# Kernel tuning notes

Hardware: AMD Instinct MI355X
Metric: run time of the kernel (lower is better)

## Reference

```python
import jax, jax.numpy as jnp
import numpy as np

H = 768; R = 16; L = 3; NS = 128; NQ = 128


def setup_inputs():
    key = jax.random.key(0)
    ks = iter(jax.random.split(key, 40))
    def w(shape, s=0.02):
        return (s * jax.random.normal(next(ks), shape)).astype(jnp.float32)
    return {
        "support_features": jax.random.normal(next(ks), (NS, H), jnp.float32),
        "support_labels": jax.random.randint(next(ks), (NS,), 0, 3),
        "query_features": jax.random.normal(next(ks), (NQ, H), jnp.float32),
        "sim_w1": w((H, 2 * H)), "sim_b1": jnp.zeros((H,), jnp.float32),
        "sim_w2": w((R, H)), "sim_b2": jnp.zeros((R,), jnp.float32),
        "div_w1": w((H, 2 * H)), "div_b1": jnp.zeros((H,), jnp.float32),
        "div_w2": w((R, H)), "div_b2": jnp.zeros((R,), jnp.float32),
        "rel_w": w((L, R, H, H)), "rel_b": jnp.zeros((L, R, H), jnp.float32),
        "agg_w1": w((L, H, 2 * H)), "agg_b1": jnp.zeros((L, H), jnp.float32),
        "agg_w2": w((L, H, H)), "agg_b2": jnp.zeros((L, H), jnp.float32),
        "ln_g": jnp.ones((L, H), jnp.float32), "ln_b": jnp.zeros((L, H), jnp.float32),
        "cls_w1": w((H // 2, H)), "cls_b1": jnp.zeros((H // 2,), jnp.float32),
        "cls_w2": w((3, H // 2)), "cls_b2": jnp.zeros((3,), jnp.float32),
    }


def _symmetrize(F):
    # torch loop fills [i,j] and [j,i] with value computed from pair (min(i,j), max(i,j)); diag stays 0
    N = F.shape[0]
    idx = jnp.arange(N)
    lower = (idx[:, None] > idx[None, :])
    Fs = jnp.where(lower[:, :, None], jnp.swapaxes(F, 0, 1), F)
    off = (idx[:, None] != idx[None, :]).astype(F.dtype)
    return Fs * off[:, :, None]


def _relations(x, w1, b1, w2, b2, diversity):
    h = x.shape[1]
    wa, wb = w1[:, :h], w1[:, h:]  # split concat([a,b]) @ w1^T into two matmuls
    pa = x @ wa.T                  # [N,H], contribution of first element (x_i)
    if diversity:
        d = jnp.abs(x[:, None, :] - x[None, :, :])   # [N,N,H]
        hid = jax.nn.relu(pa[:, None, :] + d @ wb.T + b1)
    else:
        pb = x @ wb.T
        hid = jax.nn.relu(pa[:, None, :] + pb[None, :, :] + b1)
    logits = hid @ w2.T + b2       # [N,N,R]
    return _symmetrize(jax.nn.softmax(logits, axis=-1))


def _layer_norm(y, g, b):
    mu = y.mean(-1, keepdims=True)
    var = ((y - mu) ** 2).mean(-1, keepdims=True)
    return (y - mu) / jnp.sqrt(var + 1e-5) * g + b


def _prop_layer(x, C, rw, rb, aw1, ab1, aw2, ab2, g, b):
    N = x.shape[0]
    T = jnp.einsum('jh,rkh->jrk', x, rw) + rb       # per-relation transform [N,R,H]
    msg = jnp.einsum('ijr,jrk->ik', C, T) / (N - 1)  # mean over N-1 neighbors (diag of C is 0)
    comb = jnp.concatenate([x, msg], axis=-1)
    agg = jax.nn.relu(comb @ aw1.T + ab1) @ aw2.T + ab2
    return _layer_norm(agg + x, g, b)


def reference(support_features, support_labels, query_features,
              sim_w1, sim_b1, sim_w2, sim_b2,
              div_w1, div_b1, div_w2, div_b2,
              rel_w, rel_b, agg_w1, agg_b1, agg_w2, agg_b2, ln_g, ln_b,
              cls_w1, cls_b1, cls_w2, cls_b2):
    all_x = jnp.concatenate([support_features, query_features], axis=0)
    sim = _relations(all_x, sim_w1, sim_b1, sim_w2, sim_b2, diversity=False)
    div = _relations(all_x, div_w1, div_b1, div_w2, div_b2, diversity=True)
    C = (sim + div) * 0.5
    x = all_x
    for l in range(L):
        x = _prop_layer(x, C, rel_w[l], rel_b[l], agg_w1[l], agg_b1[l],
                        agg_w2[l], agg_b2[l], ln_g[l], ln_b[l])
    q = x[support_features.shape[0]:]
    preds = jax.nn.relu(q @ cls_w1.T + cls_b1) @ cls_w2.T + cls_b2  # dropout = identity (eval)
    return preds, sim, div, x
```

## Files before the change

### kernel.cpp

```cpp
#include <hip/hip_runtime.h>
#include <hip/hip_bf16.h>
#include <hip/hip_fp16.h>


typedef __attribute__((ext_vector_type(8))) short s16x8;
typedef __attribute__((ext_vector_type(4))) float f32x4;

__device__ __forceinline__ short f2bf_s(float f){
  union { __hip_bfloat16 h; short s; } u; u.h = __float2bfloat16(f); return u.s;
}
__device__ __forceinline__ float bf_s2f(short s){
  union { __hip_bfloat16 h; short s; } u; u.s = s; return __bfloat162float(u.h);
}
__device__ __forceinline__ short f2h_s(float f){
  union { __half h; short s; } u; u.h = __float2half(f); return u.s;
}
__device__ __forceinline__ f32x4 mfma16(s16x8 a, s16x8 b, f32x4 c){
  return __builtin_amdgcn_mfma_f32_16x16x32_bf16(a, b, c, 0, 0, 0);
}
__device__ __forceinline__ f32x4 mfma16h(s16x8 a, s16x8 b, f32x4 c){
  return __builtin_amdgcn_mfma_f32_16x16x32_f16(a, b, c, 0, 0, 0);
}
__device__ __forceinline__ void gload16(void* lds, const void* g){
  __builtin_amdgcn_global_load_lds((const __attribute__((address_space(1))) void*)g,
                                   (__attribute__((address_space(3))) void*)lds,
                                   16, 0, 0);
}
__device__ __forceinline__ unsigned pack2bf(float lo, float hi){
  return __builtin_amdgcn_perm(__float_as_uint(hi), __float_as_uint(lo), 0x07060302u);
}
__device__ __forceinline__ s16x8 absdiff_h(uint4 a, uint4 b){
  union { s16x8 v; unsigned u[4]; } o;
  const unsigned au[4] = {a.x,a.y,a.z,a.w}, bu[4] = {b.x,b.y,b.z,b.w};
  #pragma unroll
  for (int w = 0; w < 4; ++w){
    unsigned d;
    asm("v_pk_add_f16 %0, %1, %2 neg_lo:[0,1] neg_hi:[0,1]"
        : "=v"(d) : "v"(au[w]), "v"(bu[w]));
    o.u[w] = d & 0x7fff7fffu;
  }
  return o.v;
}

__device__ __forceinline__ void tri_decode(int b, int& i0, int& j0){
  int jb = (int)((sqrtf(2.f*(float)b + 1.f) - 1.f)*0.5f);
  while (2*(jb+1)*(jb+2) <= b) ++jb;
  while (2*jb*(jb+1) > b) --jb;
  i0 = (b - 2*jb*(jb+1))*4;
  j0 = jb*16;
}
__device__ __forceinline__ void tri_decode8x32(int b, int& i0, int& j0){
  int jb = (int)((sqrtf(2.f*(float)b + 1.f) - 1.f)*0.5f);
  while (2*(jb+1)*(jb+2) <= b) ++jb;
  while (2*jb*(jb+1) > b) --jb;
  i0 = (b - 2*jb*(jb+1))*8;
  j0 = jb*32;
}

template<int BM, int BN, int EPI>
__global__ __launch_bounds__(256) void gemm_bt2(
    const short* __restrict__ A, int lda,
    const short* __restrict__ B, int ldb,
    float* __restrict__ Cf, short* __restrict__ Cb, int ldc,
    const float* __restrict__ bias, int K, int NT)
{
  __shared__ short As[BM*128];
  __shared__ short Bs[BN*128];
  const int tid = threadIdx.x, lane = tid & 63, wid = tid >> 6;
  const int nt = blockIdx.x % NT, mt = blockIdx.x / NT;
  const int m0 = mt*BM, n0 = nt*BN;
  const int wm0 = (wid>>1)*(BM/2), wn0 = (wid&1)*(BN/2);
  f32x4 acc[BM/32][BN/32] = {};
  for (int k0 = 0; k0 < K; k0 += 128){
    if (k0) __syncthreads();
    #pragma unroll
    for (int q = 0; q < BM/16; ++q){
      const int d = (wid*(BM/16)+q)*1024 + lane*16;
      const int row = d>>8, c = d&255;
      gload16((char*)As + (wid*(BM/16)+q)*1024,
              (const char*)A + (size_t)(m0+row)*lda*2 + (size_t)k0*2 + (c ^ ((row&7)<<4)));
    }
    #pragma unroll
    for (int q = 0; q < BN/16; ++q){
      const int d = (wid*(BN/16)+q)*1024 + lane*16;
      const int row = d>>8, c = d&255;
      gload16((char*)Bs + (wid*(BN/16)+q)*1024,
              (const char*)B + (size_t)(n0+row)*ldb*2 + (size_t)k0*2 + (c ^ ((row&7)<<4)));
    }
    __syncthreads();
    #pragma unroll
    for (int kk = 0; kk < 4; ++kk){
      const int colb = (kk*32 + (lane>>4)*8)*2;
      s16x8 af[BM/32], bfv[BN/32];
      #pragma unroll
      for (int mi = 0; mi < BM/32; ++mi){
        const int row = wm0 + mi*16 + (lane&15);
        af[mi] = *(const s16x8*)((char*)As + row*256 + (colb ^ ((row&7)<<4)));
      }
      #pragma unroll
      for (int ni = 0; ni < BN/32; ++ni){
        const int row = wn0 + ni*16 + (lane&15);
        bfv[ni] = *(const s16x8*)((char*)Bs + row*256 + (colb ^ ((row&7)<<4)));
      }
      #pragma unroll
      for (int mi = 0; mi < BM/32; ++mi)
        #pragma unroll
        for (int ni = 0; ni < BN/32; ++ni)
          acc[mi][ni] = mfma16(af[mi], bfv[ni], acc[mi][ni]);
    }
  }
  #pragma unroll
  for (int mi = 0; mi < BM/32; ++mi){
    #pragma unroll
    for (int ni = 0; ni < BN/32; ++ni){
      const int gcol = n0 + wn0 + ni*16 + (lane&15);
      const float bv = bias[gcol];
      #pragma unroll
      for (int r = 0; r < 4; ++r){
        const int grow = m0 + wm0 + mi*16 + (lane>>4)*4 + r;
        float v = acc[mi][ni][r] + bv;
        if (EPI == 2) v = fmaxf(v, 0.f);
        if (EPI == 3) Cf[(size_t)grow*ldc + gcol] = v;
        else          Cb[(size_t)grow*ldc + gcol] = f2bf_s(v);
      }
    }
  }
}

__global__ __launch_bounds__(256) void gemm_msg(
    const short* __restrict__ A,
    const short* __restrict__ B,
    float* __restrict__ slabs)
{
  __shared__ short As[64*64];
  __shared__ short Bs[64*64];
  const int tid = threadIdx.x, lane = tid & 63, wid = tid >> 6;
  const int mt = blockIdx.x / 12, nt = blockIdx.x % 12;
  const int m0 = mt*64, n0 = nt*64, kc0 = blockIdx.y*512;
  const int wm0 = (wid>>1)*32, wn0 = (wid&1)*32;
  f32x4 acc[2][2] = {};
  for (int s = 0; s < 8; ++s){
    const int k0 = kc0 + s*64;
    if (s) __syncthreads();
    #pragma unroll
    for (int q = 0; q < 2; ++q){
      const int d = (wid*2+q)*1024 + lane*16;
      const int row = d>>7, c = d&127;
      gload16((char*)As + (wid*2+q)*1024,
              (const char*)A + (size_t)(m0+row)*8192 + (size_t)k0*2 + (c ^ ((row&7)<<4)));
    }
    #pragma unroll
    for (int rd = 0; rd < 2; ++rd){
      int ei = rd*2048 + tid*8, kr = ei>>6, nc = ei&63;
      union { uint4 v; short s4[8]; } u;
      u.v = *(const uint4*)(B + (size_t)(k0+kr)*768 + n0 + nc);
      #pragma unroll
      for (int e = 0; e < 8; ++e)
        *(short*)((char*)Bs + (nc+e)*128 + ((kr*2) ^ (((nc+e)&7)<<4))) = u.s4[e];
    }
    __syncthreads();
    #pragma unroll
    for (int kk = 0; kk < 2; ++kk){
      const int colb = (kk*32 + (lane>>4)*8)*2;
      s16x8 af[2], bfv[2];
      #pragma unroll
      for (int mi = 0; mi < 2; ++mi){
        const int row = wm0 + mi*16 + (lane&15);
        af[mi] = *(const s16x8*)((char*)As + row*128 + (colb ^ ((row&7)<<4)));
      }
      #pragma unroll
      for (int ni = 0; ni < 2; ++ni){
        const int row = wn0 + ni*16 + (lane&15);
        bfv[ni] = *(const s16x8*)((char*)Bs + row*128 + (colb ^ ((row&7)<<4)));
      }
      #pragma unroll
      for (int mi = 0; mi < 2; ++mi)
        #pragma unroll
        for (int ni = 0; ni < 2; ++ni)
          acc[mi][ni] = mfma16(af[mi], bfv[ni], acc[mi][ni]);
    }
  }
  float* out = slabs + (size_t)blockIdx.y*196608;
  #pragma unroll
  for (int mi = 0; mi < 2; ++mi)
    #pragma unroll
    for (int ni = 0; ni < 2; ++ni){
      const int gcol = n0 + wn0 + ni*16 + (lane&15);
      #pragma unroll
      for (int r = 0; r < 4; ++r){
        const int grow = m0 + wm0 + mi*16 + (lane>>4)*4 + r;
        out[(size_t)grow*768 + gcol] = acc[mi][ni][r];
      }
    }
}

__global__ void msgsum(const float* __restrict__ slabs, short* __restrict__ comb){
  const int i = (blockIdx.x*256 + threadIdx.x)*4;
  if (i >= 196608) return;
  float4 s = {0.f,0.f,0.f,0.f};
  #pragma unroll
  for (int c = 0; c < 8; ++c){
    float4 v = *(const float4*)(slabs + (size_t)c*196608 + i);
    s.x += v.x; s.y += v.y; s.z += v.z; s.w += v.w;
  }
  const float sc = 1.f/255.f;
  const int row = i/768, col = i%768;
  union { uint2 u; short s4[4]; } o;
  o.s4[0]=f2bf_s(s.x*sc); o.s4[1]=f2bf_s(s.y*sc);
  o.s4[2]=f2bf_s(s.z*sc); o.s4[3]=f2bf_s(s.w*sc);
  *(uint2*)(comb + (size_t)row*1536 + 768 + col) = o.u;
}

__global__ __launch_bounds__(512, 2) void pairrel7(
    const short* __restrict__ xh,
    const short* __restrict__ wbdh,
    const float* __restrict__ P2,
    const short* __restrict__ w2d_g,
    float* __restrict__ Ldp)
{
  __shared__ short Bs[2*256*64];
  const int tid = threadIdx.x, lane = tid & 63, wv = tid >> 6;
  const int ip = wv >> 2, jj = (wv >> 1) & 1, wc = wv & 1;
  int i0, j0; tri_decode8x32(blockIdx.x, i0, j0);
  const int nt = blockIdx.y, n0 = nt*256;

  const short* xjp = xh + (size_t)(j0 + jj*16 + (lane&15))*768 + (lane>>4)*8;
  const short* xib = xh + (size_t)(i0 + 4*ip)*768 + (lane>>4)*8;

  #pragma unroll
  for (int q = 0; q < 4; ++q){
    const int d = (wv*4+q)*1024 + lane*16;
    const int row = d>>7, c = d&127;
    gload16((char*)Bs + (wv*4+q)*1024,
            (const char*)wbdh + (size_t)(n0+row)*1536 + (c ^ ((row&7)<<4)));
  }

  f32x4 acc[4][8] = {};
  for (int t = 0; t < 12; ++t){
    uint4 uja = *(const uint4*)(xjp + t*64);
    uint4 ujb = *(const uint4*)(xjp + t*64 + 32);
    uint4 uia[4], uib[4];
    #pragma unroll
    for (int mi = 0; mi < 4; ++mi){
      uia[mi] = *(const uint4*)(xib + (size_t)mi*768 + t*64);
      uib[mi] = *(const uint4*)(xib + (size_t)mi*768 + t*64 + 32);
    }
    if (t < 11){
      char* dst = (char*)Bs + ((t+1)&1)*32768;
      const char* src = (const char*)wbdh + (size_t)(t+1)*128;
      #pragma unroll
      for (int q = 0; q < 4; ++q){
        const int d = (wv*4+q)*1024 + lane*16;
        const int row = d>>7, c = d&127;
        gload16(dst + (wv*4+q)*1024, src + (size_t)(n0+row)*1536 + (c ^ ((row&7)<<4)));
      }
    }
    __builtin_amdgcn_sched_barrier(0);
    if (t < 11) asm volatile("s_waitcnt vmcnt(14)" ::: "memory");
    else        asm volatile("s_waitcnt vmcnt(10)" ::: "memory");
    __builtin_amdgcn_s_barrier();
    __builtin_amdgcn_sched_barrier(0);
    const char* bufc = (const char*)Bs + (t&1)*32768;
    #pragma unroll
    for (int kk = 0; kk < 2; ++kk){
      s16x8 af[4];
      #pragma unroll
      for (int mi = 0; mi < 4; ++mi)
        af[mi] = absdiff_h(kk ? ujb : uja, kk ? uib[mi] : uia[mi]);
      const int colb = (kk*32 + (lane>>4)*8)*2;
      #pragma unroll
      for (int ni = 0; ni < 8; ++ni){
        const int row = wc*128 + ni*16 + (lane&15);
        s16x8 bv = *(const s16x8*)(bufc + row*128 + (colb ^ ((row&7)<<4)));
        #pragma unroll
        for (int mi = 0; mi < 4; ++mi)
          acc[mi][ni] = mfma16h(af[mi], bv, acc[mi][ni]);
      }
    }
    __builtin_amdgcn_sched_barrier(0);
    __builtin_amdgcn_s_barrier();
  }
  __syncthreads();

  float* red = (float*)((char*)Bs + 32768);
  const int kh = wv >> 2, rq = wv & 3;
  #pragma unroll
  for (int h = 0; h < 4; ++h){
    if (ip == (h>>1)){
      #pragma unroll
      for (int q = 0; q < 2; ++q){
        const int mi = 2*(h&1) + q;
        const float* pr = P2 + (size_t)(i0 + 4*ip + mi)*2304 + 1536 + n0;
        #pragma unroll
        for (int ni = 0; ni < 8; ++ni){
          const int col = wc*128 + ni*16 + (lane&15);
          const float pav = pr[col];
          #pragma unroll
          for (int r = 0; r < 4; ++r){
            const int lrow = q*32 + jj*16 + (lane>>4)*4 + r;
            const float v = fmaxf(acc[mi][ni][r] + pav, 0.f);
            *(short*)((char*)Bs + lrow*512 + ((col*2) ^ ((lrow&7)<<4))) =
                (short)(__float_as_uint(v) >> 16);
          }
        }
      }
    }
    __syncthreads();
    f32x4 a2 = {0.f,0.f,0.f,0.f};
    const int arow = rq*16 + (lane&15);
    #pragma unroll
    for (int qq = 0; qq < 4; ++qq){
      const int k = kh*128 + qq*32 + (lane>>4)*8;
      s16x8 a = *(const s16x8*)((char*)Bs + arow*512 + ((k*2) ^ ((arow&7)<<4)));
      s16x8 w = *(const s16x8*)(w2d_g + (size_t)(lane&15)*768 + n0 + k);
      a2 = mfma16(a, w, a2);
    }
    if (kh == 1){
      #pragma unroll
      for (int r = 0; r < 4; ++r)
        red[(rq*16 + (lane>>4)*4 + r)*16 + (lane&15)] = a2[r];
    }
    __syncthreads();
    if (kh == 0){
      #pragma unroll
      for (int r = 0; r < 4; ++r){
        const int lrow = rq*16 + (lane>>4)*4 + r;
        const int p = h*64 + lrow;
        const int i = i0 + (p>>5), j = j0 + (p&31);
        Ldp[(size_t)nt*1048576 + (((size_t)i<<8) + j)*16 + (lane&15)]
          = a2[r] + red[lrow*16 + (lane&15)];
      }
    }
    __syncthreads();
  }
}

__global__ __launch_bounds__(256) void simpart(
    const float* __restrict__ P2,
    const short* __restrict__ w2s_g,
    float* __restrict__ Ls)
{
  __shared__ short Hs[64*256];
  const int tid = threadIdx.x, lane = tid & 63, wv = tid >> 6;
  int i0, j0; tri_decode(blockIdx.x, i0, j0);
  const int arow = wv*16 + (lane&15);
  f32x4 acc2 = {0.f,0.f,0.f,0.f};
  for (int nt = 0; nt < 3; ++nt){
    const int n0 = nt*256;
    if (nt) __syncthreads();
    {
      const int row = tid>>2, c0 = (tid&3)*64;
      const float* pap = P2 + (size_t)(i0 + (row>>4))*2304 + n0 + c0;
      const float* pbp = P2 + (size_t)(j0 + (row&15))*2304 + 768 + n0 + c0;
      #pragma unroll
      for (int cc = 0; cc < 64; cc += 8){
        float4 a0 = *(const float4*)(pap+cc), a1 = *(const float4*)(pap+cc+4);
        float4 q0 = *(const float4*)(pbp+cc), q1 = *(const float4*)(pbp+cc+4);
        uint4 o;
        o.x = pack2bf(fmaxf(a0.x+q0.x,0.f), fmaxf(a0.y+q0.y,0.f));
        o.y = pack2bf(fmaxf(a0.z+q0.z,0.f), fmaxf(a0.w+q0.w,0.f));
        o.z = pack2bf(fmaxf(a1.x+q1.x,0.f), fmaxf(a1.y+q1.y,0.f));
        o.w = pack2bf(fmaxf(a1.z+q1.z,0.f), fmaxf(a1.w+q1.w,0.f));
        *(uint4*)((char*)Hs + row*512 + (((c0+cc)*2) ^ ((row&7)<<4))) = o;
      }
    }
    __syncthreads();
    #pragma unroll
    for (int q = 0; q < 8; ++q){
      const int colb = (q*32 + (lane>>4)*8)*2;
      s16x8 a = *(const s16x8*)((const char*)Hs + arow*512 + (colb ^ ((arow&7)<<4)));
      s16x8 w = *(const s16x8*)(w2s_g + (size_t)(lane&15)*768 + n0 + q*32 + (lane>>4)*8);
      acc2 = mfma16(a, w, acc2);
    }
  }
  const int r_ = lane & 15;
  #pragma unroll
  for (int r = 0; r < 4; ++r){
    const int p = wv*16 + (lane>>4)*4 + r;
    const int i = i0 + (p>>4), j = j0 + (p&15);
    Ls[(((size_t)i<<8) + j)*16 + r_] = acc2[r];
  }
}

__global__ __launch_bounds__(256) void finisher2(
    const float* __restrict__ Ls, const float* __restrict__ Ldp,
    const float* __restrict__ b2s, const float* __restrict__ b2d,
    float* __restrict__ simo, float* __restrict__ divo, short* __restrict__ Cb)
{
  const int p = blockIdx.x*256 + threadIdx.x;
  const int i = p >> 8, j = p & 255;
  float so[16], dd[16];
  if (i == j){
    #pragma unroll
    for (int r = 0; r < 16; ++r){ so[r] = 0.f; dd[r] = 0.f; }
  } else {
    const int si = i < j ? i : j, sj = i < j ? j : i;
    const size_t base = (((size_t)si << 8) + sj) * 16;
    float mx = -1e30f, sum;
    #pragma unroll
    for (int r = 0; r < 16; ++r){ so[r] = Ls[base+r] + b2s[r]; mx = fmaxf(mx, so[r]); }
    sum = 0.f;
    #pragma unroll
    for (int r = 0; r < 16; ++r){ so[r] = expf(so[r]-mx); sum += so[r]; }
    sum = 1.f/sum;
    #pragma unroll
    for (int r = 0; r < 16; ++r) so[r] *= sum;
    mx = -1e30f;
    #pragma unroll
    for (int r = 0; r < 16; ++r){
      dd[r] = Ldp[base+r] + Ldp[base+r+1048576] + Ldp[base+r+2097152] + b2d[r];
      mx = fmaxf(mx, dd[r]);
    }
    sum = 0.f;
    #pragma unroll
    for (int r = 0; r < 16; ++r){ dd[r] = expf(dd[r]-mx); sum += dd[r]; }
    sum = 1.f/sum;
    #pragma unroll
    for (int r = 0; r < 16; ++r) dd[r] *= sum;
  }
  const size_t ob = (size_t)p * 16;
  #pragma unroll
  for (int r = 0; r < 16; ++r){
    simo[ob+r] = so[r];
    divo[ob+r] = dd[r];
    Cb[ob+r]   = f2bf_s(0.5f*(so[r]+dd[r]));
  }
}

__global__ __launch_bounds__(256) void gemm_relT(
    const short* __restrict__ A,
    const float* __restrict__ Bf,
    short* __restrict__ T,
    const float* __restrict__ bias)
{
  __shared__ short As[128*64];
  __shared__ short Bs[64*64];
  const int tid = threadIdx.x, lane = tid & 63, wv = tid >> 6;
  const int nt = blockIdx.x >> 1, mt = blockIdx.x & 1;
  const int n0 = nt*64, m0 = mt*128;
  const int wm = wv >> 1, wn = wv & 1;
  const int brow = tid >> 2, q4 = tid & 3;
  f32x4 acc[4][2] = {};
  for (int k0 = 0; k0 < 768; k0 += 64){
    if (k0) __syncthreads();
    #pragma unroll
    for (int q = 0; q < 4; ++q){
      const int d = (wv*4+q)*1024 + lane*16;
      const int row = d>>7, c = d&127;
      gload16((char*)As + (wv*4+q)*1024,
              (const char*)A + (size_t)(m0+row)*3072 + (size_t)k0*2 + (c ^ ((row&7)<<4)));
    }
    {
      const float* bp = Bf + (size_t)(n0+brow)*768 + k0 + q4*16;
      float4 v0 = *(const float4*)bp,      v1 = *(const float4*)(bp+4);
      float4 v2 = *(const float4*)(bp+8),  v3 = *(const float4*)(bp+12);
      union { uint4 v; unsigned u[4]; } ua, ub;
      ua.u[0]=pack2bf(v0.x,v0.y); ua.u[1]=pack2bf(v0.z,v0.w);
      ua.u[2]=pack2bf(v1.x,v1.y); ua.u[3]=pack2bf(v1.z,v1.w);
      ub.u[0]=pack2bf(v2.x,v2.y); ub.u[1]=pack2bf(v2.z,v2.w);
      ub.u[2]=pack2bf(v3.x,v3.y); ub.u[3]=pack2bf(v3.z,v3.w);
      const int bc = q4*32;
      *(uint4*)((char*)Bs + brow*128 + ((bc   ) ^ ((brow&7)<<4))) = ua.v;
      *(uint4*)((char*)Bs + brow*128 + ((bc+16) ^ ((brow&7)<<4))) = ub.v;
    }
    __syncthreads();
    #pragma unroll
    for (int kk = 0; kk < 2; ++kk){
      const int kb = kk*64 + (lane>>4)*16;
      s16x8 af[4], bfv[2];
      #pragma unroll
      for (int mi = 0; mi < 4; ++mi){
        const int row = wm*64 + mi*16 + (lane&15);
        af[mi] = *(const s16x8*)((char*)As + row*128 + (kb ^ ((row&7)<<4)));
      }
      #pragma unroll
      for (int ni = 0; ni < 2; ++ni){
        const int row = wn*32 + ni*16 + (lane&15);
        bfv[ni] = *(const s16x8*)((char*)Bs + row*128 + (kb ^ ((row&7)<<4)));
      }
      #pragma unroll
      for (int mi = 0; mi < 4; ++mi)
        #pragma unroll
        for (int ni = 0; ni < 2; ++ni)
          acc[mi][ni] = mfma16(af[mi], bfv[ni], acc[mi][ni]);
    }
  }
  #pragma unroll
  for (int mi = 0; mi < 4; ++mi)
    #pragma unroll
    for (int ni = 0; ni < 2; ++ni){
      const int nn = n0 + wn*32 + ni*16 + (lane&15);
      const float bv = bias[nn];
      #pragma unroll
      for (int r = 0; r < 4; ++r){
        const int row = m0 + wm*64 + mi*16 + (lane>>4)*4 + r;
        T[(size_t)row*12288 + nn] = f2bf_s(acc[mi][ni][r] + bv);
      }
    }
}

__global__ __launch_bounds__(256) void ln_kernel(
    const float* __restrict__ y, float* __restrict__ x, short* __restrict__ combx,
    const float* __restrict__ g, const float* __restrict__ b, float* __restrict__ xfinal)
{
  const int row = blockIdx.x, tid = threadIdx.x;
  float tv[3]; float s = 0.f, s2 = 0.f;
  #pragma unroll
  for (int c = 0; c < 3; ++c){
    const int idx = tid + c*256;
    const float v = y[row*768+idx] + x[row*768+idx];
    tv[c] = v; s += v; s2 += v*v;
  }
  #pragma unroll
  for (int off = 32; off > 0; off >>= 1){ s += __shfl_down(s, off); s2 += __shfl_down(s2, off); }
  __shared__ float red[8];
  const int wid = tid >> 6, lane = tid & 63;
  if (lane == 0){ red[wid] = s; red[wid+4] = s2; }
  __syncthreads();
  if (tid == 0){
    red[0] = red[0]+red[1]+red[2]+red[3];
    red[4] = red[4]+red[5]+red[6]+red[7];
  }
  __syncthreads();
  const float mu = red[0]*(1.f/768.f);
  const float var = red[4]*(1.f/768.f) - mu*mu;
  const float inv = rsqrtf(var + 1e-5f);
  #pragma unroll
  for (int c = 0; c < 3; ++c){
    const int idx = tid + c*256;
    const float v = (tv[c]-mu)*inv*g[idx] + b[idx];
    x[row*768+idx] = v;
    combx[(size_t)row*1536 + idx] = f2bf_s(v);
    if (xfinal) xfinal[row*768+idx] = v;
  }
}

__device__ __forceinline__ void cvt4(const float* __restrict__ s,
                                     short* __restrict__ d, int i, int n){
  if (i >= n) return;
  float4 v = *(const float4*)(s+i);
  union { uint2 u; short s4[4]; } o;
  o.s4[0]=f2bf_s(v.x); o.s4[1]=f2bf_s(v.y); o.s4[2]=f2bf_s(v.z); o.s4[3]=f2bf_s(v.w);
  *(uint2*)(d+i) = o.u;
}

__global__ void setup_all(
    const float* __restrict__ sim_w2, const float* __restrict__ div_w2,
    const float* __restrict__ agg_w1, const float* __restrict__ agg_w2,
    const float* __restrict__ cls_w1, const float* __restrict__ sim_w1,
    const float* __restrict__ div_w1, const float* __restrict__ sup,
    const float* __restrict__ qry, const float* __restrict__ sim_b1,
    const float* __restrict__ div_b1,
    short* __restrict__ W2S, short* __restrict__ W2D, short* __restrict__ AW1,
    short* __restrict__ AW2, short* __restrict__ CW1, short* __restrict__ W1X4,
    float* __restrict__ XF, short* __restrict__ COMB, float* __restrict__ B1C,
    short* __restrict__ XH, short* __restrict__ WBDH)
{
  const int b = blockIdx.x, tid = threadIdx.x;
  if (b < 12)        cvt4(sim_w2, W2S, (b*256+tid)*4, 12288);
  else if (b < 24)   cvt4(div_w2, W2D, ((b-12)*256+tid)*4, 12288);
  else if (b < 3480) cvt4(agg_w1, AW1, ((b-24)*256+tid)*4, 3538944);
  else if (b < 5208) cvt4(agg_w2, AW2, ((b-3480)*256+tid)*4, 1769472);
  else if (b < 5496) cvt4(cls_w1, CW1, ((b-5208)*256+tid)*4, 294912);
  else if (b < 7800){
    const int i = ((b-5496)*256+tid)*4;
    if (i < 2359296){
      const int mat = i / 589824, rem = i % 589824;
      const int r = rem / 768, c = rem % 768;
      const float* src = (mat < 2 ? sim_w1 : div_w1) + (size_t)r*1536 + (mat&1)*768 + c;
      float4 v = *(const float4*)src;
      union { uint2 u; short s4[4]; } o;
      o.s4[0]=f2bf_s(v.x); o.s4[1]=f2bf_s(v.y); o.s4[2]=f2bf_s(v.z); o.s4[3]=f2bf_s(v.w);
      *(uint2*)(W1X4+i) = o.u;
    }
  } else if (b < 7992){
    const int i = ((b-7800)*256+tid)*4;
    if (i < 196608){
      const int row = i / 768, col = i % 768;
      const float* s = (row < 128 ? sup + (size_t)row*768 : qry + (size_t)(row-128)*768) + col;
      float4 v = *(const float4*)s;
      *(float4*)(XF+i) = v;
      union { uint2 u; short s4[4]; } o;
      o.s4[0]=f2bf_s(v.x); o.s4[1]=f2bf_s(v.y); o.s4[2]=f2bf_s(v.z); o.s4[3]=f2bf_s(v.w);
      *(uint2*)(COMB + (size_t)row*1536 + col) = o.u;
      union { uint2 u; short s4[4]; } oh;
      oh.s4[0]=f2h_s(v.x); oh.s4[1]=f2h_s(v.y); oh.s4[2]=f2h_s(v.z); oh.s4[3]=f2h_s(v.w);
      *(uint2*)(XH + i) = oh.u;
    }
  } else if (b < 7993){
    for (int t = tid; t < 2304; t += 256)
      B1C[t] = (t < 768) ? sim_b1[t] : ((t < 1536) ? 0.f : div_b1[t-1536]);
  } else {
    const int i = ((b-7993)*256+tid)*4;
    if (i < 589824){
      const int r = i / 768, c = i % 768;
      float4 v = *(const float4*)(div_w1 + (size_t)r*1536 + 768 + c);
      union { uint2 u; short s4[4]; } o;
      o.s4[0]=f2h_s(v.x); o.s4[1]=f2h_s(v.y); o.s4[2]=f2h_s(v.z); o.s4[3]=f2h_s(v.w);
      *(uint2*)(WBDH + i) = o.u;
    }
  }
}

__global__ void cls2_kernel(const short* __restrict__ hc, const float* __restrict__ w2,
                            const float* __restrict__ b2, float* __restrict__ preds){
  const int t = blockIdx.x*192 + threadIdx.x;
  if (t >= 384) return;
  const int m = t/3, c = t - m*3;
  float s = b2[c];
  for (int k = 0; k < 384; ++k)
    s += bf_s2f(hc[m*384+k]) * w2[c*384+k];
  preds[m*3+c] = s;
}

static const size_t OFF_B1CAT = 0;
static const size_t OFF_LS    = 16384;
static const size_t OFF_MSGF  = 4210688;
static const size_t OFF_LDP   = 10502144;
static const size_t OFF_P     = 23085056;
static const size_t OFF_XF    = 25444352;
static const size_t OFF_Y     = 26230784;
static const size_t OFF_COMB  = 27017216;
static const size_t OFF_CB    = 27803648;
static const size_t OFF_W1X4  = 29900800;
static const size_t OFF_W2S   = 34619392;
static const size_t OFF_W2D   = 34643968;
static const size_t OFF_AW1   = 34668544;
static const size_t OFF_AW2   = 41746432;
static const size_t OFF_CW1   = 45285376;
static const size_t OFF_TBUF  = 45875200;
static const size_t OFF_HID1  = 52166656;
static const size_t OFF_HIDC  = 52559872;
static const size_t OFF_XH    = 52658176;
static const size_t OFF_WBDH  = 53051392;

extern "C" void kernel_launch(void* const* d_in, const int* in_sizes, int n_in,
                              void* d_out, int out_size, void* d_ws, size_t ws_size,
                              hipStream_t stream)
{
  (void)in_sizes; (void)n_in; (void)out_size; (void)ws_size;
  const float* sup    = (const float*)d_in[0];
  const float* qry    = (const float*)d_in[2];
  const float* sim_w1 = (const float*)d_in[3];
  const float* sim_b1 = (const float*)d_in[4];
  const float* sim_w2 = (const float*)d_in[5];
  const float* sim_b2 = (const float*)d_in[6];
  const float* div_w1 = (const float*)d_in[7];
  const float* div_b1 = (const float*)d_in[8];
  const float* div_w2 = (const float*)d_in[9];
  const float* div_b2 = (const float*)d_in[10];
  const float* rel_w  = (const float*)d_in[11];
  const float* rel_b  = (const float*)d_in[12];
  const float* agg_w1 = (const float*)d_in[13];
  const float* agg_b1 = (const float*)d_in[14];
  const float* agg_w2 = (const float*)d_in[15];
  const float* agg_b2 = (const float*)d_in[16];
  const float* ln_g   = (const float*)d_in[17];
  const float* ln_b   = (const float*)d_in[18];
  const float* cls_w1 = (const float*)d_in[19];
  const float* cls_b1 = (const float*)d_in[20];
  const float* cls_w2 = (const float*)d_in[21];
  const float* cls_b2 = (const float*)d_in[22];

  char* w = (char*)d_ws;
  float* B1C  = (float*)(w + OFF_B1CAT);
  float* LS   = (float*)(w + OFF_LS);
  float* MSGF = (float*)(w + OFF_MSGF);
  float* LDP  = (float*)(w + OFF_LDP);
  float* P2   = (float*)(w + OFF_P);
  float* XF   = (float*)(w + OFF_XF);
  float* Y    = (float*)(w + OFF_Y);
  short* COMB = (short*)(w + OFF_COMB);
  short* CB   = (short*)(w + OFF_CB);
  short* W1X4 = (short*)(w + OFF_W1X4);
  short* W2S  = (short*)(w + OFF_W2S);
  short* W2D  = (short*)(w + OFF_W2D);
  short* AW1  = (short*)(w + OFF_AW1);
  short* AW2  = (short*)(w + OFF_AW2);
  short* CW1  = (short*)(w + OFF_CW1);
  short* TBUF = (short*)(w + OFF_TBUF);
  short* HID1 = (short*)(w + OFF_HID1);
  short* HIDC = (short*)(w + OFF_HIDC);
  short* XH   = (short*)(w + OFF_XH);
  short* WBDH = (short*)(w + OFF_WBDH);

  float* preds = (float*)d_out;
  float* simo  = preds + 384;
  float* divo  = simo + 1048576;
  float* xout  = divo + 1048576;

  setup_all<<<8569, 256, 0, stream>>>(sim_w2, div_w2, agg_w1, agg_w2, cls_w1,
                                      sim_w1, div_w1, sup, qry, sim_b1, div_b1,
                                      W2S, W2D, AW1, AW2, CW1, W1X4, XF, COMB, B1C,
                                      XH, WBDH);

  gemm_bt2<64,64,3><<<144, 256, 0, stream>>>(COMB, 1536, W1X4, 768, P2, nullptr, 2304,
                                             B1C, 768, 36);

  pairrel7<<<dim3(144,3), 512, 0, stream>>>(XH, WBDH, P2, W2D, LDP);
  simpart<<<544, 256, 0, stream>>>(P2, W2S, LS);
  finisher2<<<256, 256, 0, stream>>>(LS, LDP, sim_b2, div_b2, simo, divo, CB);

  for (int l = 0; l < 3; ++l){
    gemm_relT<<<384, 256, 0, stream>>>(COMB, rel_w + (size_t)l*9437184, TBUF,
                                       rel_b + l*12288);
    gemm_msg<<<dim3(48,8), 256, 0, stream>>>(CB, TBUF, MSGF);
    msgsum<<<192, 256, 0, stream>>>(MSGF, COMB);
    gemm_bt2<32,32,2><<<192, 256, 0, stream>>>(COMB, 1536, AW1 + (size_t)l*1179648, 1536,
                                               nullptr, HID1, 768, agg_b1 + l*768, 1536, 24);
    gemm_bt2<32,32,3><<<192, 256, 0, stream>>>(HID1, 768, AW2 + (size_t)l*589824, 768,
                                               Y, nullptr, 768, agg_b2 + l*768, 768, 24);
    ln_kernel<<<256, 256, 0, stream>>>(Y, XF, COMB, ln_g + l*768, ln_b + l*768,
                                       (l == 2) ? xout : nullptr);
  }

  gemm_bt2<32,32,2><<<48, 256, 0, stream>>>(COMB + (size_t)128*1536, 1536, CW1, 768,
                                            nullptr, HIDC, 384, cls_b1, 768, 12);
  cls2_kernel<<<2, 192, 0, stream>>>(HIDC, cls_w2, cls_b2, preds);
}
```

Measured before the change: 307.8 us.

## Fuse sim logits with softmax finisher; widen relT blocks; retile P2 GEMM

The sim-part kernel now applies both softmaxes in registers, using 16-lane shuffle reductions, and writes the symmetric sim, div and C outputs directly. This removes the LS intermediate buffer and the separate finisher launch. gemm_relT now uses 512-thread blocks that each cover all 256 rows, so every rel_w tile is loaded and converted to bf16 once instead of twice. The first P2 GEMM uses a 32x64 tile with twice as many blocks, trading more redundant loads for better CU occupancy.

```diff
diff --git a/kernel.cpp b/kernel.cpp
--- a/kernel.cpp
+++ b/kernel.cpp
@@ -335,10 +335,12 @@
   }
 }
 
-__global__ __launch_bounds__(256) void simpart(
+__global__ __launch_bounds__(256) void simfused(
     const float* __restrict__ P2,
     const short* __restrict__ w2s_g,
-    float* __restrict__ Ls)
+    const float* __restrict__ Ldp,
+    const float* __restrict__ b2s, const float* __restrict__ b2d,
+    float* __restrict__ simo, float* __restrict__ divo, short* __restrict__ CBo)
 {
   __shared__ short Hs[64*256];
   const int tid = threadIdx.x, lane = tid & 63, wv = tid >> 6;
@@ -374,72 +376,53 @@
     }
   }
   const int r_ = lane & 15;
+  const float bs_ = b2s[r_], bd_ = b2d[r_];
   #pragma unroll
   for (int r = 0; r < 4; ++r){
     const int p = wv*16 + (lane>>4)*4 + r;
     const int i = i0 + (p>>4), j = j0 + (p&15);
-    Ls[(((size_t)i<<8) + j)*16 + r_] = acc2[r];
-  }
-}
-
-__global__ __launch_bounds__(256) void finisher2(
-    const float* __restrict__ Ls, const float* __restrict__ Ldp,
-    const float* __restrict__ b2s, const float* __restrict__ b2d,
-    float* __restrict__ simo, float* __restrict__ divo, short* __restrict__ Cb)
-{
-  const int p = blockIdx.x*256 + threadIdx.x;
-  const int i = p >> 8, j = p & 255;
-  float so[16], dd[16];
-  if (i == j){
-    #pragma unroll
-    for (int r = 0; r < 16; ++r){ so[r] = 0.f; dd[r] = 0.f; }
-  } else {
-    const int si = i < j ? i : j, sj = i < j ? j : i;
-    const size_t base = (((size_t)si << 8) + sj) * 16;
-    float mx = -1e30f, sum;
-    #pragma unroll
-    for (int r = 0; r < 16; ++r){ so[r] = Ls[base+r] + b2s[r]; mx = fmaxf(mx, so[r]); }
-    sum = 0.f;
-    #pragma unroll
-    for (int r = 0; r < 16; ++r){ so[r] = expf(so[r]-mx); sum += so[r]; }
-    sum = 1.f/sum;
-    #pragma unroll
-    for (int r = 0; r < 16; ++r) so[r] *= sum;
-    mx = -1e30f;
-    #pragma unroll
-    for (int r = 0; r < 16; ++r){
-      dd[r] = Ldp[base+r] + Ldp[base+r+1048576] + Ldp[base+r+2097152] + b2d[r];
-      mx = fmaxf(mx, dd[r]);
-    }
-    sum = 0.f;
-    #pragma unroll
-    for (int r = 0; r < 16; ++r){ dd[r] = expf(dd[r]-mx); sum += dd[r]; }
-    sum = 1.f/sum;
-    #pragma unroll
-    for (int r = 0; r < 16; ++r) dd[r] *= sum;
-  }
-  const size_t ob = (size_t)p * 16;
-  #pragma unroll
-  for (int r = 0; r < 16; ++r){
-    simo[ob+r] = so[r];
-    divo[ob+r] = dd[r];
-    Cb[ob+r]   = f2bf_s(0.5f*(so[r]+dd[r]));
-  }
-}
-
-__global__ __launch_bounds__(256) void gemm_relT(
+    if (j < i) continue;
+    if (j == i){
+      const size_t pii = (((size_t)i<<8) + i)*16 + r_;
+      simo[pii] = 0.f; divo[pii] = 0.f; CBo[pii] = 0;
+      continue;
+    }
+    const size_t base = (((size_t)i<<8) + j)*16;
+    const float sv = acc2[r] + bs_;
+    const float dv = Ldp[base+r_] + Ldp[base+1048576+r_] + Ldp[base+2097152+r_] + bd_;
+    float m = sv;
+    m = fmaxf(m, __shfl_xor(m,1)); m = fmaxf(m, __shfl_xor(m,2));
+    m = fmaxf(m, __shfl_xor(m,4)); m = fmaxf(m, __shfl_xor(m,8));
+    float e = expf(sv - m), s = e;
+    s += __shfl_xor(s,1); s += __shfl_xor(s,2); s += __shfl_xor(s,4); s += __shfl_xor(s,8);
+    const float so = e/s;
+    m = dv;
+    m = fmaxf(m, __shfl_xor(m,1)); m = fmaxf(m, __shfl_xor(m,2));
+    m = fmaxf(m, __shfl_xor(m,4)); m = fmaxf(m, __shfl_xor(m,8));
+    e = expf(dv - m); s = e;
+    s += __shfl_xor(s,1); s += __shfl_xor(s,2); s += __shfl_xor(s,4); s += __shfl_xor(s,8);
+    const float dd = e/s;
+    const size_t pij = base + r_;
+    const size_t pji = (((size_t)j<<8) + i)*16 + r_;
+    simo[pij] = so; simo[pji] = so;
+    divo[pij] = dd; divo[pji] = dd;
+    const short cb = f2bf_s(0.5f*(so + dd));
+    CBo[pij] = cb; CBo[pji] = cb;
+  }
+}
+
+__global__ __launch_bounds__(512) void gemm_relT(
     const short* __restrict__ A,
     const float* __restrict__ Bf,
     short* __restrict__ T,
     const float* __restrict__ bias)
 {
-  __shared__ short As[128*64];
+  __shared__ short As[256*64];
   __shared__ short Bs[64*64];
   const int tid = threadIdx.x, lane = tid & 63, wv = tid >> 6;
-  const int nt = blockIdx.x >> 1, mt = blockIdx.x & 1;
-  const int n0 = nt*64, m0 = mt*128;
+  const int n0 = blockIdx.x*64;
   const int wm = wv >> 1, wn = wv & 1;
-  const int brow = tid >> 2, q4 = tid & 3;
+  const int brow = tid >> 3, c0 = (tid & 7)*8;
   f32x4 acc[4][2] = {};
   for (int k0 = 0; k0 < 768; k0 += 64){
     if (k0) __syncthreads();
@@ -448,20 +431,15 @@
       const int d = (wv*4+q)*1024 + lane*16;
       const int row = d>>7, c = d&127;
       gload16((char*)As + (wv*4+q)*1024,
-              (const char*)A + (size_t)(m0+row)*3072 + (size_t)k0*2 + (c ^ ((row&7)<<4)));
+              (const char*)A + (size_t)row*3072 + (size_t)k0*2 + (c ^ ((row&7)<<4)));
     }
     {
-      const float* bp = Bf + (size_t)(n0+brow)*768 + k0 + q4*16;
-      float4 v0 = *(const float4*)bp,      v1 = *(const float4*)(bp+4);
-      float4 v2 = *(const float4*)(bp+8),  v3 = *(const float4*)(bp+12);
-      union { uint4 v; unsigned u[4]; } ua, ub;
-      ua.u[0]=pack2bf(v0.x,v0.y); ua.u[1]=pack2bf(v0.z,v0.w);
-      ua.u[2]=pack2bf(v1.x,v1.y); ua.u[3]=pack2bf(v1.z,v1.w);
-      ub.u[0]=pack2bf(v2.x,v2.y); ub.u[1]=pack2bf(v2.z,v2.w);
-      ub.u[2]=pack2bf(v3.x,v3.y); ub.u[3]=pack2bf(v3.z,v3.w);
-      const int bc = q4*32;
-      *(uint4*)((char*)Bs + brow*128 + ((bc   ) ^ ((brow&7)<<4))) = ua.v;
-      *(uint4*)((char*)Bs + brow*128 + ((bc+16) ^ ((brow&7)<<4))) = ub.v;
+      const float* bp = Bf + (size_t)(n0+brow)*768 + k0 + c0;
+      float4 v0 = *(const float4*)bp, v1 = *(const float4*)(bp+4);
+      union { uint4 v; unsigned u[4]; } uo;
+      uo.u[0]=pack2bf(v0.x,v0.y); uo.u[1]=pack2bf(v0.z,v0.w);
+      uo.u[2]=pack2bf(v1.x,v1.y); uo.u[3]=pack2bf(v1.z,v1.w);
+      *(uint4*)((char*)Bs + brow*128 + (((c0*2)) ^ ((brow&7)<<4))) = uo.v;
     }
     __syncthreads();
     #pragma unroll
@@ -493,7 +471,7 @@
       const float bv = bias[nn];
       #pragma unroll
       for (int r = 0; r < 4; ++r){
-        const int row = m0 + wm*64 + mi*16 + (lane>>4)*4 + r;
+        const int row = wm*64 + mi*16 + (lane>>4)*4 + r;
         T[(size_t)row*12288 + nn] = f2bf_s(acc[mi][ni][r] + bv);
       }
     }
@@ -614,7 +592,6 @@
 }
 
 static const size_t OFF_B1CAT = 0;
-static const size_t OFF_LS    = 16384;
 static const size_t OFF_MSGF  = 4210688;
 static const size_t OFF_LDP   = 10502144;
 static const size_t OFF_P     = 23085056;
@@ -664,7 +641,6 @@
 
   char* w = (char*)d_ws;
   float* B1C  = (float*)(w + OFF_B1CAT);
-  float* LS   = (float*)(w + OFF_LS);
   float* MSGF = (float*)(w + OFF_MSGF);
   float* LDP  = (float*)(w + OFF_LDP);
   float* P2   = (float*)(w + OFF_P);
@@ -694,15 +670,14 @@
                                       W2S, W2D, AW1, AW2, CW1, W1X4, XF, COMB, B1C,
                                       XH, WBDH);
 
-  gemm_bt2<64,64,3><<<144, 256, 0, stream>>>(COMB, 1536, W1X4, 768, P2, nullptr, 2304,
+  gemm_bt2<32,64,3><<<288, 256, 0, stream>>>(COMB, 1536, W1X4, 768, P2, nullptr, 2304,
                                              B1C, 768, 36);
 
   pairrel7<<<dim3(144,3), 512, 0, stream>>>(XH, WBDH, P2, W2D, LDP);
-  simpart<<<544, 256, 0, stream>>>(P2, W2S, LS);
-  finisher2<<<256, 256, 0, stream>>>(LS, LDP, sim_b2, div_b2, simo, divo, CB);
+  simfused<<<544, 256, 0, stream>>>(P2, W2S, LDP, sim_b2, div_b2, simo, divo, CB);
 
   for (int l = 0; l < 3; ++l){
-    gemm_relT<<<384, 256, 0, stream>>>(COMB, rel_w + (size_t)l*9437184, TBUF,
+    gemm_relT<<<192, 512, 0, stream>>>(COMB, rel_w + (size_t)l*9437184, TBUF,
                                        rel_b + l*12288);
     gemm_msg<<<dim3(48,8), 256, 0, stream>>>(CB, TBUF, MSGF);
     msgsum<<<192, 256, 0, stream>>>(MSGF, COMB);
```

Result: no change. 309.7 us (+0.6%).
